# Kernel optimization log

Measured on AMD Instinct MI355X. Metric: run time of the kernel, lower is better.

## Reference

```python
import jax, jax.numpy as jnp
import numpy as np

HEADS = 12
NUM_IMS = 1
SCALE = 1.0


def _layernorm(x, g, b, eps=1e-5):
    m = jnp.mean(x, axis=-1, keepdims=True)
    v = jnp.var(x, axis=-1, keepdims=True)
    return (x - m) / jnp.sqrt(v + eps) * g + b


def _mha(q, k, v):
    # q: [B, Nq, C], k/v: [B, Nk, C]; multi-head softmax attention
    B, Nq, C = q.shape
    d = C // HEADS
    qh = q.reshape(B, Nq, HEADS, d)
    kh = k.reshape(B, k.shape[1], HEADS, d)
    vh = v.reshape(B, v.shape[1], HEADS, d)
    sim = jnp.einsum('bihd,bjhd->bhij', qh, kh) * (d ** -0.5)
    w = jax.nn.softmax(sim, axis=-1)
    out = jnp.einsum('bhij,bjhd->bihd', w, vh)
    return out.reshape(B, Nq, C)


def _forward(hidden_states, encoder_hidden_states, ln1_g, ln1_b, ln2_g, ln2_b,
             sa_wq, sa_wk, sa_wv, sa_wo, sa_wo_b, ff_ln_g, ff_ln_b, ff_w1, ff_w2,
             alpha_attn, alpha_dense, ca_wq, ca_wk, ca_wv, ca_wo, ca_wo_b):
    B, N, C = hidden_states.shape
    end_pos = encoder_hidden_states.shape[1] - 16 * NUM_IMS
    text = encoder_hidden_states[:, :end_pos]   # [B, Lt, C]
    face = encoder_hidden_states[:, end_pos:]   # [B, 16, C]

    x = hidden_states
    # gated self-attention over visual tokens + face tokens
    x_ln = _layernorm(x, ln1_g, ln1_b)
    face_ln = _layernorm(face, ln1_g, ln1_b)
    comb = jnp.concatenate([x_ln, face_ln], axis=1)  # [B, N+16, C]
    attn_out = _mha(comb @ sa_wq, comb @ sa_wk, comb @ sa_wv) @ sa_wo + sa_wo_b
    attn_out = attn_out[:, :N]
    x = x + SCALE * jnp.tanh(alpha_attn) * attn_out

    # gated GEGLU feed-forward (norm2 outside, FF has its own LayerNorm)
    h = _layernorm(x, ln2_g, ln2_b)
    h = _layernorm(h, ff_ln_g, ff_ln_b)
    h = h @ ff_w1                                 # [B, N, 2*inner]
    a, gate = jnp.split(h, 2, axis=-1)
    h = (a * jax.nn.gelu(gate, approximate=False)) @ ff_w2
    x = x + SCALE * jnp.tanh(alpha_dense) * h

    residual = x
    # cross attention against text tokens (diffusers Attention, residual_connection=True)
    out = _mha(x @ ca_wq, text @ ca_wk, text @ ca_wv) @ ca_wo + ca_wo_b
    return out + residual


def setup_inputs() -> dict:
    key = jax.random.key(0)
    ks = jax.random.split(key, 16)
    B, N, C, L, INNER = 2, 1024, 768, 77 + 16 * NUM_IMS, 3072
    W = 0.02
    return {
        'hidden_states': jax.random.normal(ks[0], (B, N, C), jnp.float32),
        'encoder_hidden_states': jax.random.normal(ks[1], (B, L, C), jnp.float32),
        'ln1_g': jnp.ones((C,), jnp.float32),
        'ln1_b': jnp.zeros((C,), jnp.float32),
        'ln2_g': jnp.ones((C,), jnp.float32),
        'ln2_b': jnp.zeros((C,), jnp.float32),
        'sa_wq': jax.random.normal(ks[2], (C, C), jnp.float32) * W,
        'sa_wk': jax.random.normal(ks[3], (C, C), jnp.float32) * W,
        'sa_wv': jax.random.normal(ks[4], (C, C), jnp.float32) * W,
        'sa_wo': jax.random.normal(ks[5], (C, C), jnp.float32) * W,
        'sa_wo_b': jnp.zeros((C,), jnp.float32),
        'ff_ln_g': jnp.ones((C,), jnp.float32),
        'ff_ln_b': jnp.zeros((C,), jnp.float32),
        'ff_w1': jax.random.normal(ks[6], (C, 2 * INNER), jnp.float32) * W,
        'ff_w2': jax.random.normal(ks[7], (INNER, C), jnp.float32) * W,
        'alpha_attn': jnp.float32(0.5),
        'alpha_dense': jnp.float32(0.5),
        'ca_wq': jax.random.normal(ks[8], (C, C), jnp.float32) * W,
        'ca_wk': jax.random.normal(ks[9], (C, C), jnp.float32) * W,
        'ca_wv': jax.random.normal(ks[10], (C, C), jnp.float32) * W,
        'ca_wo': jax.random.normal(ks[11], (C, C), jnp.float32) * W,
        'ca_wo_b': jnp.zeros((C,), jnp.float32),
    }


def reference(hidden_states, encoder_hidden_states, ln1_g, ln1_b, ln2_g, ln2_b,
              sa_wq, sa_wk, sa_wv, sa_wo, sa_wo_b, ff_ln_g, ff_ln_b, ff_w1, ff_w2,
              alpha_attn, alpha_dense, ca_wq, ca_wk, ca_wv, ca_wo, ca_wo_b):
    return _forward(hidden_states, encoder_hidden_states, ln1_g, ln1_b, ln2_g, ln2_b,
                    sa_wq, sa_wk, sa_wv, sa_wo, sa_wo_b, ff_ln_g, ff_ln_b, ff_w1, ff_w2,
                    alpha_attn, alpha_dense, ca_wq, ca_wk, ca_wv, ca_wo, ca_wo_b)
```

## Files before the change

kernel.cpp:

```cpp
#include <hip/hip_runtime.h>
#include <hip/hip_bf16.h>
#include <math.h>


#define C_DIM 768
#define B_DIM 2
#define N_DIM 1024
#define NC_DIM 1040
#define L_DIM 93
#define TEXT_LEN 77
#define INNER 3072
#define MNX 1572864

typedef unsigned short ushort_t;
typedef __bf16 bf16x8 __attribute__((ext_vector_type(8)));
typedef float f32x4 __attribute__((ext_vector_type(4)));

__device__ __forceinline__ ushort_t f2b(float f) {
  __hip_bfloat16 h = __float2bfloat16(f);
  return *(ushort_t*)&h;
}
__device__ __forceinline__ float b2f(ushort_t u) {
  __hip_bfloat16 h = *(__hip_bfloat16*)&u;
  return __bfloat162float(h);
}

__device__ __forceinline__ void g2lds16(const void* g, void* l) {
  __builtin_amdgcn_global_load_lds(
      (const __attribute__((address_space(1))) unsigned int*)g,
      (__attribute__((address_space(3))) unsigned int*)l, 16, 0, 0);
}

#define WX1    0u
#define WX2    6291456u
#define WQKV   12582912u
#define WBB1   22167552u
#define WG     47333376u
#define WS1    59916288u
#define WTEXT  63062016u
#define WATT2  63298560u
#define WWQKV  66444288u
#define WWO    69983232u
#define WW1    71162880u
#define WW2    80600064u
#define WCAWQ  85318656u
#define WCAKV  86498304u
#define WCAWO  88857600u
#define WVT1   90037248u
#define WVT2   93379584u
#define WOPART WBB1
#define WLBUF  WG
#define WATTN  (WG + 524288u)
#define WPART  WBB1

__device__ __forceinline__ float block_sum(float v, float* sh) {
#pragma unroll
  for (int o = 32; o > 0; o >>= 1) v += __shfl_down(v, o);
  int lane = threadIdx.x & 63, w = threadIdx.x >> 6;
  if (lane == 0) sh[w] = v;
  __syncthreads();
  float r = sh[0] + sh[1] + sh[2] + sh[3];
  __syncthreads();
  return r;
}

struct WtDesc {
  const float* src[10];
  ushort_t*    dst[10];
  int K[10];
  int N[10];
  int tilesX[10];
  int ileave[10];
  int start[11];
};

__global__ __launch_bounds__(256)
void wtrans_batched(WtDesc d) {
  __shared__ float tile[64][65];
  int bid = blockIdx.x;
  int j = 0;
  while (j < 9 && bid >= d.start[j + 1]) ++j;
  int ti = bid - d.start[j];
  int K = d.K[j], N = d.N[j];
  int n0 = (ti % d.tilesX[j]) * 64, k0 = (ti / d.tilesX[j]) * 64;
  const float* in = d.src[j];
  ushort_t* out = d.dst[j];
  int il = d.ileave[j];
  int t = threadIdx.x;
#pragma unroll
  for (int p = 0; p < 16; ++p) {
    int idx = t + p * 256;
    int r = idx >> 6, c = idx & 63;
    tile[r][c] = in[(size_t)(k0 + r) * N + n0 + c];
  }
  __syncthreads();
#pragma unroll
  for (int p = 0; p < 16; ++p) {
    int idx = t + p * 256;
    int r = idx >> 6, c = idx & 63;
    int nrow = n0 + r;
    int dstrow = il ? ((nrow < INNER) ? (nrow * 2) : ((nrow - INNER) * 2 + 1)) : nrow;
    out[(size_t)dstrow * K + k0 + c] = f2b(tile[c][r]);
  }
}

__global__ __launch_bounds__(256)
void ln_concat_kernel(const float* __restrict__ x, const float* __restrict__ enc,
                      const float* __restrict__ g, const float* __restrict__ b,
                      ushort_t* __restrict__ comb, ushort_t* __restrict__ text) {
  __shared__ float sh[4];
  int r = blockIdx.x;
  if (r >= B_DIM * NC_DIM) {
    int i = r - B_DIM * NC_DIM;
    int bb = i / TEXT_LEN, j = i % TEXT_LEN;
    const float* src = enc + ((size_t)bb * L_DIM + j) * C_DIM;
    ushort_t* dst = text + (size_t)i * C_DIM;
#pragma unroll
    for (int l = 0; l < 3; ++l) {
      int c = threadIdx.x + l * 256;
      dst[c] = f2b(src[c]);
    }
    return;
  }
  int bb = r / NC_DIM, i = r % NC_DIM;
  const float* src = (i < N_DIM)
      ? (x   + ((size_t)bb * N_DIM + i) * C_DIM)
      : (enc + ((size_t)bb * L_DIM + TEXT_LEN + (i - N_DIM)) * C_DIM);
  float v[3];
#pragma unroll
  for (int j = 0; j < 3; ++j) v[j] = src[threadIdx.x + j * 256];
  float mean = block_sum(v[0] + v[1] + v[2], sh) * (1.f / C_DIM);
  float sq = 0.f;
#pragma unroll
  for (int j = 0; j < 3; ++j) { float d = v[j] - mean; sq += d * d; }
  float rstd = rsqrtf(block_sum(sq, sh) * (1.f / C_DIM) + 1e-5f);
  ushort_t* dst = comb + (size_t)r * C_DIM;
#pragma unroll
  for (int j = 0; j < 3; ++j) {
    int c = threadIdx.x + j * 256;
    dst[c] = f2b((v[j] - mean) * rstd * g[c] + b[c]);
  }
}

__global__ __launch_bounds__(256)
void gemm_bf16(const ushort_t* __restrict__ A, const ushort_t* __restrict__ Bt,
               ushort_t* __restrict__ Ob, ushort_t* __restrict__ Og,
               int M, int N, int K) {
  __shared__ ushort_t sA[2][128 * 32];
  __shared__ ushort_t sB[2][128 * 32];
  int t = threadIdx.x;
  int w = t >> 6, ln = t & 63;
  int m0 = blockIdx.y * 128, n0 = blockIdx.x * 128;
  int wm = (w >> 1) * 64, wn = (w & 1) * 64;
  int lr = ln & 15, lq = ln >> 4;
  int seg_r = ln >> 2, seg_c = (ln & 3) * 8;

  f32x4 acc[4][4];
#pragma unroll
  for (int mi = 0; mi < 4; ++mi)
#pragma unroll
    for (int ni = 0; ni < 4; ++ni) acc[mi][ni] = (f32x4){0.f, 0.f, 0.f, 0.f};

#define STAGE(k0_, buf_)                                                     \
  do {                                                                       \
    _Pragma("unroll") for (int l = 0; l < 2; ++l) {                          \
      int s = w * 2 + l;                                                     \
      int arow = m0 + s * 16 + seg_r;                                        \
      arow = arow < M ? arow : M - 1;                                        \
      g2lds16(A + (size_t)arow * K + (k0_) + seg_c, &sA[buf_][s * 512]);     \
      int nrow = n0 + s * 16 + seg_r;                                        \
      g2lds16(Bt + (size_t)nrow * K + (k0_) + seg_c, &sB[buf_][s * 512]);    \
    }                                                                        \
  } while (0)

  STAGE(0, 0);
  __syncthreads();
  int cur = 0;
  for (int k0 = 0; k0 < K; k0 += 32) {
    if (k0 + 32 < K) STAGE(k0 + 32, cur ^ 1);
    bf16x8 af[4], bfr[4];
#pragma unroll
    for (int mi = 0; mi < 4; ++mi)
      af[mi] = *(const bf16x8*)&sA[cur][(wm + mi * 16 + lr) * 32 + lq * 8];
#pragma unroll
    for (int ni = 0; ni < 4; ++ni)
      bfr[ni] = *(const bf16x8*)&sB[cur][(wn + ni * 16 + lr) * 32 + lq * 8];
#pragma unroll
    for (int mi = 0; mi < 4; ++mi)
#pragma unroll
      for (int ni = 0; ni < 4; ++ni)
        acc[mi][ni] = __builtin_amdgcn_mfma_f32_16x16x32_bf16(
            af[mi], bfr[ni], acc[mi][ni], 0, 0, 0);
    __syncthreads();
    cur ^= 1;
  }
#undef STAGE

  if (Og) {
#pragma unroll
    for (int mi = 0; mi < 4; ++mi)
#pragma unroll
      for (int ni = 0; ni < 4; ++ni) {
        int col = n0 + wn + ni * 16 + lr;
#pragma unroll
        for (int r = 0; r < 4; ++r) {
          float val = acc[mi][ni][r];
          float other = __shfl_xor(val, 1);
          if (!(lr & 1)) {
            float a = val, gate = other;
            float ge = 0.5f * gate * (1.f + erff(gate * 0.70710678118654752f));
            int row = m0 + wm + mi * 16 + lq * 4 + r;
            Og[(size_t)row * INNER + (col >> 1)] = f2b(a * ge);
          }
        }
      }
  } else {
#pragma unroll
    for (int mi = 0; mi < 4; ++mi)
#pragma unroll
      for (int ni = 0; ni < 4; ++ni) {
        int col = n0 + wn + ni * 16 + lr;
#pragma unroll
        for (int r = 0; r < 4; ++r) {
          int row = m0 + wm + mi * 16 + lq * 4 + r;
          if (row < M) Ob[(size_t)row * N + col] = f2b(acc[mi][ni][r]);
        }
      }
  }
}

__global__ __launch_bounds__(256)
void gemm64(const ushort_t* __restrict__ A, const ushort_t* __restrict__ Bt,
            float* __restrict__ Out, ushort_t* __restrict__ Ob,
            float* __restrict__ Part,
            int M, int N, int K, int Ksplit,
            const float* __restrict__ bias, const float* __restrict__ res,
            const float* __restrict__ alphaPtr) {
  __shared__ ushort_t sA[2][4096];
  __shared__ ushort_t sB[2][4096];
  int t = threadIdx.x;
  int w = t >> 6, ln = t & 63;
  int m0 = blockIdx.y * 64, n0 = blockIdx.x * 64;
  int wm = (w >> 1) * 32, wn = (w & 1) * 32;
  int lr = ln & 15, lq = ln >> 4;
  int srow = (w & 1) * 32 + (ln >> 2);
  int skoff = (w >> 1) * 32 + (ln & 3) * 8;
  int kbeg = blockIdx.z * Ksplit;
  int kend = kbeg + Ksplit; if (kend > K) kend = K;

  f32x4 acc[2][2];
#pragma unroll
  for (int mi = 0; mi < 2; ++mi)
#pragma unroll
    for (int ni = 0; ni < 2; ++ni) acc[mi][ni] = (f32x4){0.f, 0.f, 0.f, 0.f};

#define STG64(k0_, buf_)                                                      \
  do {                                                                        \
    _Pragma("unroll") for (int i = 0; i < 2; ++i) {                           \
      int ar = m0 + srow + i * 16; ar = ar < M ? ar : M - 1;                  \
      g2lds16(A + (size_t)ar * K + (k0_) + skoff,                             \
              (char*)sA + (buf_) * 8192 + w * 2048 + i * 1024);               \
      int nr = n0 + srow + i * 16;                                            \
      g2lds16(Bt + (size_t)nr * K + (k0_) + skoff,                            \
              (char*)sB + (buf_) * 8192 + w * 2048 + i * 1024);               \
    }                                                                         \
  } while (0)

  STG64(kbeg, 0);
  __syncthreads();
  int cur = 0;
  for (int k0 = kbeg; k0 < kend; k0 += 64) {
    if (k0 + 64 < kend) STG64(k0 + 64, cur ^ 1);
#pragma unroll
    for (int s = 0; s < 2; ++s) {
      bf16x8 a0 = *(const bf16x8*)&sA[cur][s * 2048 + (wm + lr) * 32 + lq * 8];
      bf16x8 a1 = *(const bf16x8*)&sA[cur][s * 2048 + (wm + 16 + lr) * 32 + lq * 8];
      bf16x8 b0 = *(const bf16x8*)&sB[cur][s * 2048 + (wn + lr) * 32 + lq * 8];
      bf16x8 b1 = *(const bf16x8*)&sB[cur][s * 2048 + (wn + 16 + lr) * 32 + lq * 8];
      acc[0][0] = __builtin_amdgcn_mfma_f32_16x16x32_bf16(a0, b0, acc[0][0], 0, 0, 0);
      acc[0][1] = __builtin_amdgcn_mfma_f32_16x16x32_bf16(a0, b1, acc[0][1], 0, 0, 0);
      acc[1][0] = __builtin_amdgcn_mfma_f32_16x16x32_bf16(a1, b0, acc[1][0], 0, 0, 0);
      acc[1][1] = __builtin_amdgcn_mfma_f32_16x16x32_bf16(a1, b1, acc[1][1], 0, 0, 0);
    }
    __syncthreads();
    cur ^= 1;
  }
#undef STG64

  if (Part) {
    float* P = Part + (size_t)blockIdx.z * M * N;
#pragma unroll
    for (int mi = 0; mi < 2; ++mi)
#pragma unroll
      for (int ni = 0; ni < 2; ++ni) {
        int col = n0 + wn + ni * 16 + lr;
#pragma unroll
        for (int r = 0; r < 4; ++r) {
          int row = m0 + wm + mi * 16 + lq * 4 + r;
          if (row < M) P[(size_t)row * N + col] = acc[mi][ni][r];
        }
      }
  } else {
    float f = alphaPtr ? tanhf(alphaPtr[0]) : 1.0f;
#pragma unroll
    for (int mi = 0; mi < 2; ++mi)
#pragma unroll
      for (int ni = 0; ni < 2; ++ni) {
        int col = n0 + wn + ni * 16 + lr;
        float bv = bias ? bias[col] : 0.f;
#pragma unroll
        for (int r = 0; r < 4; ++r) {
          int row = m0 + wm + mi * 16 + lq * 4 + r;
          if (row < M) {
            float val = acc[mi][ni][r] + bv;
            if (res) val = res[(size_t)row * N + col] + f * val;
            if (Out) Out[(size_t)row * N + col] = val;
            if (Ob)  Ob[(size_t)row * N + col] = f2b(val);
          }
        }
      }
  }
}

__global__ __launch_bounds__(256)
void splitk_epi(const float* __restrict__ Part, int nz, float* __restrict__ Out,
                ushort_t* __restrict__ Ob, int MN, int N,
                const float* __restrict__ bias, const float* __restrict__ res,
                const float* __restrict__ alphaPtr) {
  int idx = (blockIdx.x * 256 + threadIdx.x) * 4;
  if (idx >= MN) return;
  float f = alphaPtr ? tanhf(alphaPtr[0]) : 1.0f;
  float v[4] = {0.f, 0.f, 0.f, 0.f};
  for (int z = 0; z < nz; ++z) {
    float4 a = *(const float4*)&Part[(size_t)z * MN + idx];
    v[0] += a.x; v[1] += a.y; v[2] += a.z; v[3] += a.w;
  }
  if (bias) {
    int col = idx % N;
    float4 bb = *(const float4*)&bias[col];
    v[0] += bb.x; v[1] += bb.y; v[2] += bb.z; v[3] += bb.w;
  }
  if (res) {
    float4 rr = *(const float4*)&res[idx];
    v[0] = rr.x + f * v[0]; v[1] = rr.y + f * v[1];
    v[2] = rr.z + f * v[2]; v[3] = rr.w + f * v[3];
  }
  if (Out) *(float4*)&Out[idx] = make_float4(v[0], v[1], v[2], v[3]);
  if (Ob) {
    ushort4 o;
    o.x = f2b(v[0]); o.y = f2b(v[1]); o.z = f2b(v[2]); o.w = f2b(v[3]);
    *(ushort4*)&Ob[idx] = o;
  }
}

__global__ __launch_bounds__(256)
void woepi_ln_kernel(const float* __restrict__ Part, int nz,
                     const float* __restrict__ bias, const float* __restrict__ xres,
                     const float* __restrict__ alphaPtr, float* __restrict__ x1,
                     const float* __restrict__ g1, const float* __restrict__ b1,
                     const float* __restrict__ g2, const float* __restrict__ b2,
                     ushort_t* __restrict__ hh) {
  __shared__ float sh[4];
  int row = blockIdx.x;
  float f = tanhf(alphaPtr[0]);
  float v[3];
#pragma unroll
  for (int j = 0; j < 3; ++j) {
    int c = threadIdx.x + j * 256;
    float s = 0.f;
    for (int z = 0; z < nz; ++z) s += Part[(size_t)z * MNX + (size_t)row * C_DIM + c];
    s += bias[c];
    float xv = xres[(size_t)row * C_DIM + c] + f * s;
    x1[(size_t)row * C_DIM + c] = xv;
    v[j] = xv;
  }
  float mean = block_sum(v[0] + v[1] + v[2], sh) * (1.f / C_DIM);
  float sq = 0.f;
#pragma unroll
  for (int j = 0; j < 3; ++j) { float d = v[j] - mean; sq += d * d; }
  float rstd = rsqrtf(block_sum(sq, sh) * (1.f / C_DIM) + 1e-5f);
  float y[3];
#pragma unroll
  for (int j = 0; j < 3; ++j) {
    int c = threadIdx.x + j * 256;
    y[j] = (v[j] - mean) * rstd * g1[c] + b1[c];
  }
  float mean2 = block_sum(y[0] + y[1] + y[2], sh) * (1.f / C_DIM);
  sq = 0.f;
#pragma unroll
  for (int j = 0; j < 3; ++j) { float d = y[j] - mean2; sq += d * d; }
  float rstd2 = rsqrtf(block_sum(sq, sh) * (1.f / C_DIM) + 1e-5f);
#pragma unroll
  for (int j = 0; j < 3; ++j) {
    int c = threadIdx.x + j * 256;
    hh[(size_t)row * C_DIM + c] = f2b((y[j] - mean2) * rstd2 * g2[c] + b2[c]);
  }
}

__global__ __launch_bounds__(256)
void vtrans_kernel(const ushort_t* __restrict__ V, ushort_t* __restrict__ Vt,
                   int rows_per_b, int stride, int Nk, int Nkp) {
  __shared__ ushort_t tile[64][68];
  int k0 = blockIdx.x * 64;
  int h = blockIdx.y, b = blockIdx.z;
  int t = threadIdx.x;
#pragma unroll
  for (int p = 0; p < 4; ++p) {
    int r = p * 16 + (t >> 4), c = (t & 15) * 4;
    int key = k0 + r;
    ushort4 u = make_ushort4(0, 0, 0, 0);
    if (key < Nk)
      u = *(const ushort4*)&V[((size_t)(b * rows_per_b + key)) * stride + h * 64 + c];
    *(ushort4*)&tile[r][c] = u;
  }
  __syncthreads();
  size_t base = ((size_t)(b * 12 + h)) * 64 * Nkp;
#pragma unroll
  for (int p = 0; p < 4; ++p) {
    int dv = p * 16 + (t >> 4), kc = (t & 15) * 4;
    ushort4 u;
    u.x = tile[kc + 0][dv]; u.y = tile[kc + 1][dv];
    u.z = tile[kc + 2][dv]; u.w = tile[kc + 3][dv];
    *(ushort4*)&Vt[base + (size_t)dv * Nkp + k0 + kc] = u;
  }
}

__global__ __launch_bounds__(256)
void attn_mfma(const ushort_t* __restrict__ Q, const ushort_t* __restrict__ K,
               const ushort_t* __restrict__ Vt, ushort_t* __restrict__ O,
               float* __restrict__ Opart, float* __restrict__ lbuf,
               int q_rows_per_b, int kv_rows_per_b, int Nk, int Nkp,
               int qstride, int kstride, int nchunk) {
  __shared__ ushort_t sQ[4096];
  __shared__ ushort_t sK[2][4096];
  __shared__ ushort_t sV[2][4096];
  __shared__ ushort_t sP[4][1024];
  const float scale = 0.18033688011112042f;
  const float M0 = 16.0f;
  int t = threadIdx.x;
  int w = t >> 6, ln = t & 63;
  int col = ln & 15, quad = ln >> 4;
  int z = blockIdx.z;
  int b = z / nchunk, kc = z % nchunk;
  int h = blockIdx.y, q0 = blockIdx.x * 64;
  size_t vt_base = ((size_t)(b * 12 + h)) * 64 * Nkp;
  int ntiles = Nkp >> 6;
  int t0 = (kc * ntiles) / nchunk;
  int t1 = ((kc + 1) * ntiles) / nchunk;

#define STAGE_KV(kt_, bb_)                                                    \
  do {                                                                        \
    _Pragma("unroll") for (int s = 0; s < 2; ++s) {                           \
      int key = (kt_) * 64 + w * 16 + (ln >> 2);                              \
      g2lds16(K + (size_t)(b * kv_rows_per_b + key) * kstride                 \
                + h * 64 + s * 32 + (ln & 3) * 8,                             \
              (char*)sK[bb_] + s * 4096 + w * 1024);                          \
      int dv = w * 16 + (ln >> 2);                                            \
      g2lds16(Vt + vt_base + (size_t)dv * Nkp                                 \
                + (kt_) * 64 + s * 32 + (ln & 3) * 8,                         \
              (char*)sV[bb_] + s * 4096 + w * 1024);                          \
    }                                                                         \
  } while (0)

#pragma unroll
  for (int s = 0; s < 2; ++s) {
    int r = q0 + w * 16 + (ln >> 2);
    g2lds16(Q + (size_t)(b * q_rows_per_b + r) * qstride + h * 64 + s * 32 + (ln & 3) * 8,
            (char*)sQ + s * 4096 + w * 1024);
  }
  STAGE_KV(t0, 0);
  __syncthreads();
  bf16x8 qa[2];
#pragma unroll
  for (int s = 0; s < 2; ++s)
    qa[s] = *(const bf16x8*)&sQ[s * 2048 + (w * 16 + col) * 32 + quad * 8];

  f32x4 oacc[4];
#pragma unroll
  for (int i = 0; i < 4; ++i) oacc[i] = (f32x4){0.f, 0.f, 0.f, 0.f};
  float l_i[4] = {0.f, 0.f, 0.f, 0.f};

  ushort_t* sPw = sP[w];
  int bb = 0;

  for (int kt = t0; kt < t1; ++kt) {
    if (kt + 1 < t1) STAGE_KV(kt + 1, bb ^ 1);

    f32x4 cs[4];
#pragma unroll
    for (int nblk = 0; nblk < 4; ++nblk) {
      cs[nblk] = (f32x4){0.f, 0.f, 0.f, 0.f};
#pragma unroll
      for (int s = 0; s < 2; ++s) {
        bf16x8 kb = *(const bf16x8*)&sK[bb][s * 2048 + (nblk * 16 + col) * 32 + quad * 8];
        cs[nblk] = __builtin_amdgcn_mfma_f32_16x16x32_bf16(qa[s], kb, cs[nblk], 0, 0, 0);
      }
    }
    if (kt * 64 + 64 > Nk) {
#pragma unroll
      for (int nblk = 0; nblk < 4; ++nblk) {
        bool valid = (kt * 64 + nblk * 16 + col) < Nk;
#pragma unroll
        for (int r = 0; r < 4; ++r)
          cs[nblk][r] = valid ? cs[nblk][r] : -1e30f;
      }
    }
#pragma unroll
    for (int r = 0; r < 4; ++r) {
      int row = quad * 4 + r;
#pragma unroll
      for (int nblk = 0; nblk < 4; ++nblk) {
        float p = exp2f(fmaf(cs[nblk][r], scale, -M0));
        l_i[r] += p;
        int kin = (nblk & 1) * 16 + col;
        sPw[(nblk >> 1) * 512 + row * 32 + (kin ^ (quad << 3))] = f2b(p);
      }
    }
#pragma unroll
    for (int s = 0; s < 2; ++s) {
      bf16x8 pa = *(const bf16x8*)&sPw[s * 512 + col * 32 + ((quad ^ ((col >> 2) & 3)) << 3)];
#pragma unroll
      for (int nblk = 0; nblk < 4; ++nblk) {
        bf16x8 vb = *(const bf16x8*)&sV[bb][s * 2048 + (nblk * 16 + col) * 32 + quad * 8];
        oacc[nblk] = __builtin_amdgcn_mfma_f32_16x16x32_bf16(pa, vb, oacc[nblk], 0, 0, 0);
      }
    }
    if (kt + 1 < t1) __syncthreads();
    bb ^= 1;
  }
#undef STAGE_KV

#pragma unroll
  for (int r = 0; r < 4; ++r) {
    float ps = l_i[r];
#pragma unroll
    for (int o = 1; o < 16; o <<= 1) ps += __shfl_xor(ps, o);
    int qglob = b * N_DIM + q0 + w * 16 + quad * 4 + r;
    if (Opart) {
      if (col == 0) lbuf[(size_t)kc * (B_DIM * N_DIM * 12) + (size_t)qglob * 12 + h] = ps;
      float* op = Opart + (size_t)kc * MNX + (size_t)qglob * C_DIM + h * 64;
#pragma unroll
      for (int nblk = 0; nblk < 4; ++nblk)
        op[nblk * 16 + col] = oacc[nblk][r];
    } else {
      float inv = 1.f / ps;
#pragma unroll
      for (int nblk = 0; nblk < 4; ++nblk)
        O[(size_t)qglob * C_DIM + h * 64 + nblk * 16 + col] = f2b(oacc[nblk][r] * inv);
    }
  }
}

__global__ __launch_bounds__(256)
void attn_merge(const float* __restrict__ Opart, const float* __restrict__ lbuf,
                ushort_t* __restrict__ Ob, int nchunk) {
  int idx = (blockIdx.x * 256 + threadIdx.x) * 4;
  if (idx >= MNX) return;
  int row = idx / C_DIM, c = idx % C_DIM;
  int h = c >> 6;
  float l = 0.f;
  float v[4] = {0.f, 0.f, 0.f, 0.f};
  for (int kc = 0; kc < nchunk; ++kc) {
    l += lbuf[(size_t)kc * (B_DIM * N_DIM * 12) + (size_t)row * 12 + h];
    float4 p = *(const float4*)&Opart[(size_t)kc * MNX + idx];
    v[0] += p.x; v[1] += p.y; v[2] += p.z; v[3] += p.w;
  }
  float inv = 1.f / l;
  ushort4 o;
  o.x = f2b(v[0] * inv); o.y = f2b(v[1] * inv);
  o.z = f2b(v[2] * inv); o.w = f2b(v[3] * inv);
  *(ushort4*)&Ob[idx] = o;
}

extern "C" void kernel_launch(void* const* d_in, const int* in_sizes, int n_in,
                              void* d_out, int out_size, void* d_ws, size_t ws_size,
                              hipStream_t stream) {
  const float* x        = (const float*)d_in[0];
  const float* enc      = (const float*)d_in[1];
  const float* ln1_g    = (const float*)d_in[2];
  const float* ln1_b    = (const float*)d_in[3];
  const float* ln2_g    = (const float*)d_in[4];
  const float* ln2_b    = (const float*)d_in[5];
  const float* sa_wq    = (const float*)d_in[6];
  const float* sa_wk    = (const float*)d_in[7];
  const float* sa_wv    = (const float*)d_in[8];
  const float* sa_wo    = (const float*)d_in[9];
  const float* sa_wo_b  = (const float*)d_in[10];
  const float* ff_ln_g  = (const float*)d_in[11];
  const float* ff_ln_b  = (const float*)d_in[12];
  const float* ff_w1    = (const float*)d_in[13];
  const float* ff_w2    = (const float*)d_in[14];
  const float* a_attn   = (const float*)d_in[15];
  const float* a_dense  = (const float*)d_in[16];
  const float* ca_wq    = (const float*)d_in[17];
  const float* ca_wk    = (const float*)d_in[18];
  const float* ca_wv    = (const float*)d_in[19];
  const float* ca_wo    = (const float*)d_in[20];
  const float* ca_wo_b  = (const float*)d_in[21];

  char* ws = (char*)d_ws;
  float*    x1     = (float*)(ws + WX1);
  float*    x2     = (float*)(ws + WX2);
  ushort_t* qkv_b  = (ushort_t*)(ws + WQKV);
  ushort_t* q2b    = (ushort_t*)(ws + WQKV);
  ushort_t* kv2b   = (ushort_t*)(ws + WQKV + 3145728u);
  ushort_t* comb_b = (ushort_t*)(ws + WBB1);
  float*    opart  = (float*)(ws + WOPART);
  float*    lbuf   = (float*)(ws + WLBUF);
  ushort_t* attn_b = (ushort_t*)(ws + WATTN);
  ushort_t* g_b    = (ushort_t*)(ws + WG);
  ushort_t* hh     = (ushort_t*)(ws + WS1);
  ushort_t* x2b    = (ushort_t*)(ws + WS1);
  ushort_t* text_b = (ushort_t*)(ws + WTEXT);
  ushort_t* attn2b = (ushort_t*)(ws + WATT2);
  ushort_t* wqkv_t = (ushort_t*)(ws + WWQKV);
  ushort_t* wo_t   = (ushort_t*)(ws + WWO);
  ushort_t* w1_t   = (ushort_t*)(ws + WW1);
  ushort_t* w2_t   = (ushort_t*)(ws + WW2);
  ushort_t* cawq_t = (ushort_t*)(ws + WCAWQ);
  ushort_t* cakv_t = (ushort_t*)(ws + WCAKV);
  ushort_t* cawo_t = (ushort_t*)(ws + WCAWO);
  ushort_t* vt1    = (ushort_t*)(ws + WVT1);
  ushort_t* vt2    = (ushort_t*)(ws + WVT2);
  float* part = (float*)(ws + WPART);
  float* out = (float*)d_out;

  const int Mc = B_DIM * NC_DIM;
  const int Mx = B_DIM * N_DIM;
  const int Mt = B_DIM * TEXT_LEN;

  WtDesc wd;
  const float* srcs[10] = {sa_wq, sa_wk, sa_wv, sa_wo, ca_wq, ca_wk, ca_wv, ca_wo, ff_w1, ff_w2};
  ushort_t* dsts[10] = {wqkv_t, wqkv_t + 589824, wqkv_t + 2 * 589824, wo_t,
                        cawq_t, cakv_t, cakv_t + 589824, cawo_t, w1_t, w2_t};
  int Ks[10] = {768, 768, 768, 768, 768, 768, 768, 768, 768, 3072};
  int Ns[10] = {768, 768, 768, 768, 768, 768, 768, 768, 6144, 768};
  int total = 0;
  for (int j = 0; j < 10; ++j) {
    wd.src[j] = srcs[j]; wd.dst[j] = dsts[j];
    wd.K[j] = Ks[j]; wd.N[j] = Ns[j];
    wd.tilesX[j] = Ns[j] / 64;
    wd.ileave[j] = (j == 8) ? 1 : 0;
    wd.start[j] = total;
    total += (Ns[j] / 64) * (Ks[j] / 64);
  }
  wd.start[10] = total;

  wtrans_batched<<<total, 256, 0, stream>>>(wd);
  ln_concat_kernel<<<Mc + Mt, 256, 0, stream>>>(x, enc, ln1_g, ln1_b, comb_b, text_b);
  gemm64<<<dim3(36, 33, 1), 256, 0, stream>>>(
      comb_b, wqkv_t, nullptr, qkv_b, nullptr, Mc, 2304, 768, 768,
      nullptr, nullptr, nullptr);
  vtrans_kernel<<<dim3(17, 12, B_DIM), 256, 0, stream>>>(
      qkv_b + 1536, vt1, NC_DIM, 2304, NC_DIM, 1088);
  attn_mfma<<<dim3(N_DIM / 64, 12, B_DIM * 2), 256, 0, stream>>>(
      qkv_b + 0, qkv_b + 768, vt1, nullptr, opart, lbuf,
      NC_DIM, NC_DIM, NC_DIM, 1088, 2304, 2304, 2);
  attn_merge<<<MNX / 1024, 256, 0, stream>>>(opart, lbuf, attn_b, 2);
  gemm64<<<dim3(12, 32, 2), 256, 0, stream>>>(
      attn_b, wo_t, nullptr, nullptr, part, Mx, 768, 768, 384,
      nullptr, nullptr, nullptr);
  woepi_ln_kernel<<<Mx, 256, 0, stream>>>(
      part, 2, sa_wo_b, x, a_attn, x1, ln2_g, ln2_b, ff_ln_g, ff_ln_b, hh);
  gemm_bf16<<<dim3(48, 16), 256, 0, stream>>>(
      hh, w1_t, nullptr, g_b, Mx, 6144, 768);
  gemm64<<<dim3(12, 32, 4), 256, 0, stream>>>(
      g_b, w2_t, nullptr, nullptr, part, Mx, 768, 3072, 768,
      nullptr, nullptr, nullptr);
  splitk_epi<<<MNX / 1024, 256, 0, stream>>>(
      part, 4, x2, x2b, MNX, 768, nullptr, x1, a_dense);
  gemm64<<<dim3(12, 32, 2), 256, 0, stream>>>(
      x2b, cawq_t, nullptr, nullptr, part, Mx, 768, 768, 384,
      nullptr, nullptr, nullptr);
  splitk_epi<<<MNX / 1024, 256, 0, stream>>>(
      part, 2, nullptr, q2b, MNX, 768, nullptr, nullptr, nullptr);
  gemm64<<<dim3(24, 3, 1), 256, 0, stream>>>(
      text_b, cakv_t, nullptr, kv2b, nullptr, Mt, 1536, 768, 768,
      nullptr, nullptr, nullptr);
  vtrans_kernel<<<dim3(2, 12, B_DIM), 256, 0, stream>>>(
      kv2b + 768, vt2, TEXT_LEN, 1536, TEXT_LEN, 128);
  attn_mfma<<<dim3(N_DIM / 64, 12, B_DIM), 256, 0, stream>>>(
      q2b, kv2b + 0, vt2, attn2b, nullptr, nullptr,
      N_DIM, TEXT_LEN, TEXT_LEN, 128, 768, 1536, 1);
  gemm64<<<dim3(12, 32, 2), 256, 0, stream>>>(
      attn2b, cawo_t, nullptr, nullptr, part, Mx, 768, 768, 384,
      nullptr, nullptr, nullptr);
  splitk_epi<<<MNX / 1024, 256, 0, stream>>>(
      part, 2, out, nullptr, MNX, 768, ca_wo_b, x2, nullptr);
}
```

Before: 322.5 us.

## Merge prep kernels, batch cross-attn KV with QKV GEMM, drop split-K passes

Folds the weight transpose and LayerNorm/concat into one prep launch. The text K/V projection and its V transpose now ride as extra blocks inside the self-attention QKV GEMM and V-transpose launches. The FF2 GEMM drops from split-K 4 to 2. The cross-attention Q and output GEMMs run without split-K, writing directly with a fused bias/residual epilogue, which removes two splitk_epi launches. Fewer launches and fewer partial-sum round trips, at the cost of less parallelism per GEMM (384 blocks) and some branch divergence in the merged kernels.

```diff
diff --git a/kernel.cpp b/kernel.cpp
--- a/kernel.cpp
+++ b/kernel.cpp
@@ -75,9 +75,48 @@
 };
 
 __global__ __launch_bounds__(256)
-void wtrans_batched(WtDesc d) {
+void prep_kernel(WtDesc d,
+                 const float* __restrict__ x, const float* __restrict__ enc,
+                 const float* __restrict__ g, const float* __restrict__ b,
+                 ushort_t* __restrict__ comb, ushort_t* __restrict__ text) {
   __shared__ float tile[64][65];
   int bid = blockIdx.x;
+  int nwt = d.start[10];
+  if (bid >= nwt) {
+    int r = bid - nwt;
+    if (r >= B_DIM * NC_DIM) {
+      int i = r - B_DIM * NC_DIM;
+      int bb = i / TEXT_LEN, j = i % TEXT_LEN;
+      const float* src = enc + ((size_t)bb * L_DIM + j) * C_DIM;
+      ushort_t* dst = text + (size_t)i * C_DIM;
+#pragma unroll
+      for (int l = 0; l < 3; ++l) {
+        int c = threadIdx.x + l * 256;
+        dst[c] = f2b(src[c]);
+      }
+      return;
+    }
+    float* sh = &tile[0][0];
+    int bb = r / NC_DIM, i = r % NC_DIM;
+    const float* src = (i < N_DIM)
+        ? (x   + ((size_t)bb * N_DIM + i) * C_DIM)
+        : (enc + ((size_t)bb * L_DIM + TEXT_LEN + (i - N_DIM)) * C_DIM);
+    float v[3];
+#pragma unroll
+    for (int j = 0; j < 3; ++j) v[j] = src[threadIdx.x + j * 256];
+    float mean = block_sum(v[0] + v[1] + v[2], sh) * (1.f / C_DIM);
+    float sq = 0.f;
+#pragma unroll
+    for (int j = 0; j < 3; ++j) { float dd = v[j] - mean; sq += dd * dd; }
+    float rstd = rsqrtf(block_sum(sq, sh) * (1.f / C_DIM) + 1e-5f);
+    ushort_t* dst = comb + (size_t)r * C_DIM;
+#pragma unroll
+    for (int j = 0; j < 3; ++j) {
+      int c = threadIdx.x + j * 256;
+      dst[c] = f2b((v[j] - mean) * rstd * g[c] + b[c]);
+    }
+    return;
+  }
   int j = 0;
   while (j < 9 && bid >= d.start[j + 1]) ++j;
   int ti = bid - d.start[j];
@@ -101,44 +140,6 @@
     int nrow = n0 + r;
     int dstrow = il ? ((nrow < INNER) ? (nrow * 2) : ((nrow - INNER) * 2 + 1)) : nrow;
     out[(size_t)dstrow * K + k0 + c] = f2b(tile[c][r]);
-  }
-}
-
-__global__ __launch_bounds__(256)
-void ln_concat_kernel(const float* __restrict__ x, const float* __restrict__ enc,
-                      const float* __restrict__ g, const float* __restrict__ b,
-                      ushort_t* __restrict__ comb, ushort_t* __restrict__ text) {
-  __shared__ float sh[4];
-  int r = blockIdx.x;
-  if (r >= B_DIM * NC_DIM) {
-    int i = r - B_DIM * NC_DIM;
-    int bb = i / TEXT_LEN, j = i % TEXT_LEN;
-    const float* src = enc + ((size_t)bb * L_DIM + j) * C_DIM;
-    ushort_t* dst = text + (size_t)i * C_DIM;
-#pragma unroll
-    for (int l = 0; l < 3; ++l) {
-      int c = threadIdx.x + l * 256;
-      dst[c] = f2b(src[c]);
-    }
-    return;
-  }
-  int bb = r / NC_DIM, i = r % NC_DIM;
-  const float* src = (i < N_DIM)
-      ? (x   + ((size_t)bb * N_DIM + i) * C_DIM)
-      : (enc + ((size_t)bb * L_DIM + TEXT_LEN + (i - N_DIM)) * C_DIM);
-  float v[3];
-#pragma unroll
-  for (int j = 0; j < 3; ++j) v[j] = src[threadIdx.x + j * 256];
-  float mean = block_sum(v[0] + v[1] + v[2], sh) * (1.f / C_DIM);
-  float sq = 0.f;
-#pragma unroll
-  for (int j = 0; j < 3; ++j) { float d = v[j] - mean; sq += d * d; }
-  float rstd = rsqrtf(block_sum(sq, sh) * (1.f / C_DIM) + 1e-5f);
-  ushort_t* dst = comb + (size_t)r * C_DIM;
-#pragma unroll
-  for (int j = 0; j < 3; ++j) {
-    int c = threadIdx.x + j * 256;
-    dst[c] = f2b((v[j] - mean) * rstd * g[c] + b[c]);
   }
 }
 
@@ -235,12 +236,21 @@
             float* __restrict__ Part,
             int M, int N, int K, int Ksplit,
             const float* __restrict__ bias, const float* __restrict__ res,
-            const float* __restrict__ alphaPtr) {
+            const float* __restrict__ alphaPtr,
+            const ushort_t* __restrict__ A2, const ushort_t* __restrict__ Bt2,
+            ushort_t* __restrict__ Ob2, int M2, int N2, int ybreak) {
   __shared__ ushort_t sA[2][4096];
   __shared__ ushort_t sB[2][4096];
+  int by = blockIdx.y;
+  if (A2 && by >= ybreak) {
+    if ((int)blockIdx.x * 64 >= N2) return;
+    A = A2; Bt = Bt2; Ob = Ob2; M = M2; N = N2;
+    Out = nullptr; Part = nullptr; bias = nullptr; res = nullptr; alphaPtr = nullptr;
+    by -= ybreak;
+  }
   int t = threadIdx.x;
   int w = t >> 6, ln = t & 63;
-  int m0 = blockIdx.y * 64, n0 = blockIdx.x * 64;
+  int m0 = by * 64, n0 = blockIdx.x * 64;
   int wm = (w >> 1) * 32, wn = (w & 1) * 32;
   int lr = ln & 15, lq = ln >> 4;
   int srow = (w & 1) * 32 + (ln >> 2);
@@ -399,9 +409,16 @@
 
 __global__ __launch_bounds__(256)
 void vtrans_kernel(const ushort_t* __restrict__ V, ushort_t* __restrict__ Vt,
-                   int rows_per_b, int stride, int Nk, int Nkp) {
+                   int rows_per_b, int stride, int Nk, int Nkp,
+                   const ushort_t* __restrict__ V2, ushort_t* __restrict__ Vt2,
+                   int rows2, int stride2, int Nk2, int Nkp2, int xbreak) {
   __shared__ ushort_t tile[64][68];
-  int k0 = blockIdx.x * 64;
+  int bx = blockIdx.x;
+  if (bx >= xbreak) {
+    bx -= xbreak;
+    V = V2; Vt = Vt2; rows_per_b = rows2; stride = stride2; Nk = Nk2; Nkp = Nkp2;
+  }
+  int k0 = bx * 64;
   int h = blockIdx.y, b = blockIdx.z;
   int t = threadIdx.x;
 #pragma unroll
@@ -646,45 +663,42 @@
   }
   wd.start[10] = total;
 
-  wtrans_batched<<<total, 256, 0, stream>>>(wd);
-  ln_concat_kernel<<<Mc + Mt, 256, 0, stream>>>(x, enc, ln1_g, ln1_b, comb_b, text_b);
-  gemm64<<<dim3(36, 33, 1), 256, 0, stream>>>(
+  prep_kernel<<<total + Mc + Mt, 256, 0, stream>>>(
+      wd, x, enc, ln1_g, ln1_b, comb_b, text_b);
+  gemm64<<<dim3(36, 36, 1), 256, 0, stream>>>(
       comb_b, wqkv_t, nullptr, qkv_b, nullptr, Mc, 2304, 768, 768,
-      nullptr, nullptr, nullptr);
-  vtrans_kernel<<<dim3(17, 12, B_DIM), 256, 0, stream>>>(
-      qkv_b + 1536, vt1, NC_DIM, 2304, NC_DIM, 1088);
+      nullptr, nullptr, nullptr,
+      text_b, cakv_t, kv2b, Mt, 1536, 33);
+  vtrans_kernel<<<dim3(19, 12, B_DIM), 256, 0, stream>>>(
+      qkv_b + 1536, vt1, NC_DIM, 2304, NC_DIM, 1088,
+      kv2b + 768, vt2, TEXT_LEN, 1536, TEXT_LEN, 128, 17);
   attn_mfma<<<dim3(N_DIM / 64, 12, B_DIM * 2), 256, 0, stream>>>(
       qkv_b + 0, qkv_b + 768, vt1, nullptr, opart, lbuf,
       NC_DIM, NC_DIM, NC_DIM, 1088, 2304, 2304, 2);
   attn_merge<<<MNX / 1024, 256, 0, stream>>>(opart, lbuf, attn_b, 2);
   gemm64<<<dim3(12, 32, 2), 256, 0, stream>>>(
       attn_b, wo_t, nullptr, nullptr, part, Mx, 768, 768, 384,
-      nullptr, nullptr, nullptr);
+      nullptr, nullptr, nullptr,
+      nullptr, nullptr, nullptr, 0, 0, 0);
   woepi_ln_kernel<<<Mx, 256, 0, stream>>>(
       part, 2, sa_wo_b, x, a_attn, x1, ln2_g, ln2_b, ff_ln_g, ff_ln_b, hh);
   gemm_bf16<<<dim3(48, 16), 256, 0, stream>>>(
       hh, w1_t, nullptr, g_b, Mx, 6144, 768);
-  gemm64<<<dim3(12, 32, 4), 256, 0, stream>>>(
-      g_b, w2_t, nullptr, nullptr, part, Mx, 768, 3072, 768,
-      nullptr, nullptr, nullptr);
+  gemm64<<<dim3(12, 32, 2), 256, 0, stream>>>(
+      g_b, w2_t, nullptr, nullptr, part, Mx, 768, 3072, 1536,
+      nullptr, nullptr, nullptr,
+      nullptr, nullptr, nullptr, 0, 0, 0);
   splitk_epi<<<MNX / 1024, 256, 0, stream>>>(
-      part, 4, x2, x2b, MNX, 768, nullptr, x1, a_dense);
-  gemm64<<<dim3(12, 32, 2), 256, 0, stream>>>(
-      x2b, cawq_t, nullptr, nullptr, part, Mx, 768, 768, 384,
-      nullptr, nullptr, nullptr);
-  splitk_epi<<<MNX / 1024, 256, 0, stream>>>(
-      part, 2, nullptr, q2b, MNX, 768, nullptr, nullptr, nullptr);
-  gemm64<<<dim3(24, 3, 1), 256, 0, stream>>>(
-      text_b, cakv_t, nullptr, kv2b, nullptr, Mt, 1536, 768, 768,
-      nullptr, nullptr, nullptr);
-  vtrans_kernel<<<dim3(2, 12, B_DIM), 256, 0, stream>>>(
-      kv2b + 768, vt2, TEXT_LEN, 1536, TEXT_LEN, 128);
+      part, 2, x2, x2b, MNX, 768, nullptr, x1, a_dense);
+  gemm64<<<dim3(12, 32, 1), 256, 0, stream>>>(
+      x2b, cawq_t, nullptr, q2b, nullptr, Mx, 768, 768, 768,
+      nullptr, nullptr, nullptr,
+      nullptr, nullptr, nullptr, 0, 0, 0);
   attn_mfma<<<dim3(N_DIM / 64, 12, B_DIM), 256, 0, stream>>>(
       q2b, kv2b + 0, vt2, attn2b, nullptr, nullptr,
       N_DIM, TEXT_LEN, TEXT_LEN, 128, 768, 1536, 1);
-  gemm64<<<dim3(12, 32, 2), 256, 0, stream>>>(
-      attn2b, cawo_t, nullptr, nullptr, part, Mx, 768, 768, 384,
-      nullptr, nullptr, nullptr);
-  splitk_epi<<<MNX / 1024, 256, 0, stream>>>(
-      part, 2, out, nullptr, MNX, 768, ca_wo_b, x2, nullptr);
-}
+  gemm64<<<dim3(12, 32, 1), 256, 0, stream>>>(
+      attn2b, cawo_t, out, nullptr, nullptr, Mx, 768, 768, 768,
+      ca_wo_b, x2, nullptr,
+      nullptr, nullptr, nullptr, 0, 0, 0);
+}
```

Measured after the change: 304.5 us. 5.6% less time.
